# Kernel tuning notes

Hardware: AMD Instinct MI355X
Metric: run time of the kernel (lower is better)

Reference implementation:

```python
import jax, jax.numpy as jnp
import numpy as np

B, M, C, S, SD, K, H = 32, 448, 384, 512, 128, 8, 8
DH = C // H
EPS = 1e-5
NEG_SLOPE = 0.2


def setup_inputs() -> dict:
    key = jax.random.key(0)
    ks = iter(jax.random.split(key, 32))
    nrm = lambda shape, scale=0.05: (jax.random.normal(next(ks), shape, jnp.float32) * scale)
    inp = {
        'q': jax.random.normal(next(ks), (B, M, C), jnp.float32),
        'coarse': jax.random.normal(next(ks), (B, M, 3), jnp.float32),
        'skeleton': jax.random.normal(next(ks), (B, S, 3), jnp.float32),
        # GraphConv 1: 3 -> 64 (root weight, rel/neighbor weight, bias)
        'gc1_wroot': nrm((3, 64), 0.3), 'gc1_wrel': nrm((3, 64), 0.3), 'gc1_b': jnp.zeros((64,), jnp.float32),
        # GraphConv 2: 64 -> SD
        'gc2_wroot': nrm((64, SD), 0.1), 'gc2_wrel': nrm((64, SD), 0.1), 'gc2_b': jnp.zeros((SD,), jnp.float32),
        # skeleton_projection: SD -> C
        'proj_w': nrm((SD, C), 0.08), 'proj_b': jnp.zeros((C,), jnp.float32),
        # MultiheadAttention (torch layout: in_proj (3C, C), out_proj (C, C))
        'attn_in_w': nrm((3 * C, C), 0.05), 'attn_in_b': jnp.zeros((3 * C,), jnp.float32),
        'attn_out_w': nrm((C, C), 0.05), 'attn_out_b': jnp.zeros((C,), jnp.float32),
        # increase_dim: Conv1d(C,1024,1) + BN(1024) + LeakyReLU + Conv1d(1024,1024,1)
        'inc1_w': nrm((1024, C), 0.05), 'inc1_b': jnp.zeros((1024,), jnp.float32),
        'bn_g': jnp.ones((1024,), jnp.float32), 'bn_b': jnp.zeros((1024,), jnp.float32),
        'bn_m': jnp.zeros((1024,), jnp.float32), 'bn_v': jnp.ones((1024,), jnp.float32),
        'inc2_w': nrm((1024, 1024), 0.03), 'inc2_b': jnp.zeros((1024,), jnp.float32),
        # reduce_map: Linear(C + 1024 + 3, C)
        'red_w': nrm((1024 + C + 3, C), 0.03), 'red_b': jnp.zeros((C,), jnp.float32),
    }
    return inp


def _knn_idx(pts):
    # pts: [B,S,3]; per-batch kNN (self excluded), matching knn_graph(k=K, batch=...)
    d2 = jnp.sum((pts[:, :, None, :] - pts[:, None, :, :]) ** 2, axis=-1)  # [B,S,S]
    d2 = d2 + jnp.eye(S, dtype=pts.dtype)[None] * 1e10                       # mask self
    _, idx = jax.lax.top_k(-d2, K)                                           # [B,S,K]
    return idx


def _graph_conv(x, idx, wroot, wrel, b):
    # GraphConv (PyG, aggr='add'): out_i = x_i Wroot + (sum_{j in N(i)} x_j) Wrel + b
    nb = jax.vmap(lambda f, i: f[i])(x, idx)   # [B,S,K,F]
    agg = nb.sum(axis=2)                       # [B,S,F]
    return x @ wroot + agg @ wrel + b


def reference(q, coarse, skeleton, gc1_wroot, gc1_wrel, gc1_b, gc2_wroot, gc2_wrel, gc2_b,
              proj_w, proj_b, attn_in_w, attn_in_b, attn_out_w, attn_out_b,
              inc1_w, inc1_b, bn_g, bn_b, bn_m, bn_v, inc2_w, inc2_b, red_w, red_b):
    # --- skeleton branch: knn graph + 2-layer GraphConv + max-pool + projection ---
    idx = _knn_idx(skeleton)
    h = _graph_conv(skeleton, idx, gc1_wroot, gc1_wrel, gc1_b)
    h = jax.nn.relu(h)
    h = _graph_conv(h, idx, gc2_wroot, gc2_wrel, gc2_b)        # [B,S,SD]
    proxy = jnp.max(h, axis=1)                                  # [B,SD]
    proxy = proxy @ proj_w + proj_b                             # [B,C]
    kv = jnp.broadcast_to(proxy[:, None, :], (B, M, C))         # expanded proxies

    # --- cross attention (torch nn.MultiheadAttention math) ---
    wq, wk, wv = attn_in_w[:C], attn_in_w[C:2 * C], attn_in_w[2 * C:]
    bq, bk, bv = attn_in_b[:C], attn_in_b[C:2 * C], attn_in_b[2 * C:]
    qh = (q @ wq.T + bq).reshape(B, M, H, DH)
    kh = (kv @ wk.T + bk).reshape(B, M, H, DH)
    vh = (kv @ wv.T + bv).reshape(B, M, H, DH)
    scores = jnp.einsum('bmhd,bnhd->bhmn', qh, kh) / jnp.sqrt(jnp.float32(DH))
    attn = jax.nn.softmax(scores, axis=-1)
    ctx = jnp.einsum('bhmn,bnhd->bmhd', attn, vh).reshape(B, M, C)
    q = ctx @ attn_out_w.T + attn_out_b                         # fused features [B,M,C]

    # --- increase_dim (1x1 conv == matmul) + BN(eval) + LeakyReLU + 1x1 conv ---
    g = jnp.einsum('bmc,oc->bmo', q, inc1_w) + inc1_b           # [B,M,1024]
    g = bn_g * (g - bn_m) * jax.lax.rsqrt(bn_v + EPS) + bn_b
    g = jnp.where(g >= 0, g, NEG_SLOPE * g)
    g = jnp.einsum('bmc,oc->bmo', g, inc2_w) + inc2_b
    global_feature = jnp.max(g, axis=1)                         # [B,1024]

    # --- concat + reduce_map ---
    rebuild = jnp.concatenate([jnp.broadcast_to(global_feature[:, None, :], (B, M, 1024)), q, coarse], axis=-1)
    out = rebuild @ red_w + red_b                               # [B,M,C]
    return out
```

## Files before the change

kernel.cpp:

```cpp
#include <hip/hip_runtime.h>

#define NB 32
#define MM 448
#define CC 384
#define SS 512
#define KNN 8

#define WS_IDX   0u
#define WS_H1    524288u
#define WS_PMAX  (WS_H1 + 4194304u)
#define WS_Q     (WS_PMAX + 262144u)
#define WS_Y     (WS_Q + 49152u)
#define WS_G2    (WS_Y + 131072u)
#define WS_BASEP (WS_G2 + 131072u)
#define WS_PP    WS_H1

__device__ __forceinline__ float wave_sum(float v) {
#pragma unroll
  for (int m = 1; m < 64; m <<= 1) v += __shfl_xor(v, m, 64);
  return v;
}

__global__ __launch_bounds__(256) void k_knn_gc1(
    const float* __restrict__ skel,
    const float* __restrict__ w1root, const float* __restrict__ w1rel,
    const float* __restrict__ b1,
    int* __restrict__ idx_ws, float* __restrict__ h1_ws)
{
  int b   = blockIdx.x >> 7;
  int grp = blockIdx.x & 127;
  __shared__ __align__(16) float4 sk[SS];
  const float* sb = skel + b * SS * 3;
  for (int t = threadIdx.x; t < SS; t += 256)
    sk[t] = make_float4(sb[t*3+0], sb[t*3+1], sb[t*3+2], 0.f);
  __syncthreads();

  int wave = threadIdx.x >> 6, lane = threadIdx.x & 63;
  int i = grp * 4 + wave;
  float4 pi = sk[i];

  float bd[KNN];
#pragma unroll
  for (int t = 0; t < KNN; t++) {
    int j = lane + (t << 6);
    float4 p = sk[j];
    float d2;
    {
#pragma clang fp contract(off)
      float dx = pi.x - p.x, dy = pi.y - p.y, dz = pi.z - p.z;
      d2 = (dx*dx + dy*dy) + dz*dz;
    }
    bd[t] = (j == i) ? 3e38f : d2;
  }

  int win[KNN];
  int* idx_base = idx_ws + (size_t)(b*SS + i) * KNN;
#pragma unroll
  for (int t = 0; t < KNN; t++) {
    float bestd = bd[0]; int bests = 0;
#pragma unroll
    for (int s = 1; s < KNN; s++)
      if (bd[s] < bestd) { bestd = bd[s]; bests = s; }
    int bestj = lane + (bests << 6);
#pragma unroll
    for (int m = 1; m < 64; m <<= 1) {
      float od = __shfl_xor(bestd, m, 64);
      int   oj = __shfl_xor(bestj, m, 64);
      if (od < bestd || (od == bestd && oj < bestj)) { bestd = od; bestj = oj; }
    }
    win[t] = bestj;
    if (lane == t) idx_base[t] = bestj;
    if ((bestj & 63) == lane) {
      int sl = bestj >> 6;
#pragma unroll
      for (int s = 0; s < KNN; s++) if (s == sl) bd[s] = 3e38f;
    }
  }

  float a0 = 0.f, a1 = 0.f, a2 = 0.f;
#pragma unroll
  for (int t = 0; t < KNN; t++) {
    float4 n = sk[win[t]];
    a0 += n.x; a1 += n.y; a2 += n.z;
  }

  int c = lane;
  float h = b1[c] + pi.x*w1root[c] + pi.y*w1root[64+c] + pi.z*w1root[128+c]
                  + a0*w1rel[c]   + a1*w1rel[64+c]   + a2*w1rel[128+c];
  h = fmaxf(h, 0.f);
  h1_ws[(size_t)(b*SS + i) * 64 + lane] = h;
}

__global__ __launch_bounds__(256) void k_gc2_max(
    const float* __restrict__ h1_ws, const int* __restrict__ idx_ws,
    const float* __restrict__ w2root, const float* __restrict__ w2rel,
    const float* __restrict__ b2, float* __restrict__ pmax)
{
  int b = blockIdx.x >> 4, chunk = blockIdx.x & 15;
  int r0 = chunk * 32;
  __shared__ __align__(16) float X[32*129];
  __shared__ __align__(16) float Wt[32*128];
  __shared__ float mred[8*128];
  __shared__ int nbs[32*KNN];

  const float* h1b = h1_ws + (size_t)b * SS * 64;
  nbs[threadIdx.x] = idx_ws[(b*SS + r0)*KNN + threadIdx.x];
#pragma unroll
  for (int p = 0; p < 8; p++) {
    int idx = threadIdx.x + 256*p;
    int r = idx >> 6, k = idx & 63;
    X[r*129 + k] = h1b[(r0 + r)*64 + k];
  }
  __syncthreads();
#pragma unroll
  for (int p = 0; p < 8; p++) {
    int idx = threadIdx.x + 256*p;
    int r = idx >> 6, k = idx & 63;
    const int* nb = nbs + r*KNN;
    float s = 0.f;
#pragma unroll
    for (int j = 0; j < KNN; j++) s += h1b[nb[j]*64 + k];
    X[r*129 + 64 + k] = s;
  }

  int rg = threadIdx.x >> 5, cg = threadIdx.x & 31;
  float acc[4][4];
#pragma unroll
  for (int r = 0; r < 4; r++)
#pragma unroll
    for (int u = 0; u < 4; u++) acc[r][u] = 0.f;

  const float* wsrc[4] = { w2root, w2root + 32*128, w2rel, w2rel + 32*128 };
#pragma unroll 1
  for (int ch = 0; ch < 4; ch++) {
    __syncthreads();
    const float* ws = wsrc[ch];
#pragma unroll
    for (int p = 0; p < 16; p++) {
      int idx = threadIdx.x + 256*p;
      Wt[idx] = ws[idx];
    }
    __syncthreads();
    int kb = ch * 32;
    const float* xr0 = X + (rg*4+0)*129 + kb;
    const float* xr1 = X + (rg*4+1)*129 + kb;
    const float* xr2 = X + (rg*4+2)*129 + kb;
    const float* xr3 = X + (rg*4+3)*129 + kb;
#pragma unroll 4
    for (int k = 0; k < 32; k++) {
      float4 w4 = *(const float4*)(Wt + k*128 + cg*4);
      float x0 = xr0[k], x1 = xr1[k], x2 = xr2[k], x3 = xr3[k];
      acc[0][0] += x0*w4.x; acc[0][1] += x0*w4.y; acc[0][2] += x0*w4.z; acc[0][3] += x0*w4.w;
      acc[1][0] += x1*w4.x; acc[1][1] += x1*w4.y; acc[1][2] += x1*w4.z; acc[1][3] += x1*w4.w;
      acc[2][0] += x2*w4.x; acc[2][1] += x2*w4.y; acc[2][2] += x2*w4.z; acc[2][3] += x2*w4.w;
      acc[3][0] += x3*w4.x; acc[3][1] += x3*w4.y; acc[3][2] += x3*w4.z; acc[3][3] += x3*w4.w;
    }
  }
#pragma unroll
  for (int u = 0; u < 4; u++)
    mred[rg*128 + cg*4 + u] =
      fmaxf(fmaxf(acc[0][u], acc[1][u]), fmaxf(acc[2][u], acc[3][u]));
  __syncthreads();
  if (threadIdx.x < 128) {
    int col = threadIdx.x;
    float mx = mred[col];
#pragma unroll
    for (int g = 1; g < 8; g++) mx = fmaxf(mx, mred[g*128 + col]);
    pmax[(size_t)(b*16 + chunk)*128 + col] = mx + b2[col];
  }
}

__global__ __launch_bounds__(384) void k_attn_chain(
    const float* __restrict__ pmax,
    const float* __restrict__ proj_w, const float* __restrict__ proj_b,
    const float* __restrict__ attn_in_w, const float* __restrict__ attn_in_b,
    const float* __restrict__ attn_out_w, const float* __restrict__ attn_out_b,
    float* __restrict__ q_ws)
{
  int b = blockIdx.x, t = threadIdx.x;
  __shared__ float proxy[128];
  __shared__ float kv[CC];
  __shared__ float vv[CC];
  if (t < 128) {
    float m = -3e38f;
    for (int ch = 0; ch < 16; ch++) m = fmaxf(m, pmax[(size_t)(b*16 + ch)*128 + t]);
    proxy[t] = m;
  }
  __syncthreads();
  {
    float acc = proj_b[t];
    for (int s = 0; s < 128; s++) acc += proxy[s] * proj_w[s*CC + t];
    kv[t] = acc;
  }
  __syncthreads();
  int wv = t >> 6, lane = t & 63;
  {
    float x0 = kv[lane*6+0], x1 = kv[lane*6+1], x2 = kv[lane*6+2];
    float x3 = kv[lane*6+3], x4 = kv[lane*6+4], x5 = kv[lane*6+5];
#pragma unroll 8
    for (int u = 0; u < 64; u++) {
      int o = wv*64 + u;
      const float* wr = attn_in_w + (size_t)(2*CC + o) * CC + lane*6;
      float2 wa = *(const float2*)wr;
      float2 wb = *(const float2*)(wr + 2);
      float2 wc = *(const float2*)(wr + 4);
      float p = wa.x*x0 + wa.y*x1 + wb.x*x2 + wb.y*x3 + wc.x*x4 + wc.y*x5;
      p = wave_sum(p);
      if (lane == 0) vv[o] = attn_in_b[2*CC + o] + p;
    }
  }
  __syncthreads();
  {
    float x0 = vv[lane*6+0], x1 = vv[lane*6+1], x2 = vv[lane*6+2];
    float x3 = vv[lane*6+3], x4 = vv[lane*6+4], x5 = vv[lane*6+5];
#pragma unroll 8
    for (int u = 0; u < 64; u++) {
      int o = wv*64 + u;
      const float* wr = attn_out_w + (size_t)o * CC + lane*6;
      float2 wa = *(const float2*)wr;
      float2 wb = *(const float2*)(wr + 2);
      float2 wc = *(const float2*)(wr + 4);
      float p = wa.x*x0 + wa.y*x1 + wb.x*x2 + wb.y*x3 + wc.x*x4 + wc.y*x5;
      p = wave_sum(p);
      if (lane == 0) q_ws[b*CC + o] = attn_out_b[o] + p;
    }
  }
}

__global__ __launch_bounds__(256) void k_inc1_bn(
    const float* __restrict__ q_ws, const float* __restrict__ inc1_w,
    const float* __restrict__ inc1_b,
    const float* __restrict__ bng, const float* __restrict__ bnb,
    const float* __restrict__ bnm, const float* __restrict__ bnv,
    float* __restrict__ y_ws)
{
  int b = blockIdx.x >> 5, og = blockIdx.x & 31;
  int wv = threadIdx.x >> 6, lane = threadIdx.x & 63;
  __shared__ float xs[CC];
  for (int t = threadIdx.x; t < CC; t += 256) xs[t] = q_ws[b*CC + t];
  __syncthreads();
  float x0 = xs[lane*6+0], x1 = xs[lane*6+1], x2 = xs[lane*6+2];
  float x3 = xs[lane*6+3], x4 = xs[lane*6+4], x5 = xs[lane*6+5];
#pragma unroll
  for (int u = 0; u < 8; u++) {
    int o = og*32 + wv*8 + u;
    const float* wr = inc1_w + (size_t)o * CC + lane*6;
    float2 wa = *(const float2*)wr;
    float2 wb = *(const float2*)(wr + 2);
    float2 wc = *(const float2*)(wr + 4);
    float p = wa.x*x0 + wa.y*x1 + wb.x*x2 + wb.y*x3 + wc.x*x4 + wc.y*x5;
    p = wave_sum(p);
    if (lane == 0) {
      float acc = p + inc1_b[o];
      float z = bng[o] * (acc - bnm[o]) * rsqrtf(bnv[o] + 1e-5f) + bnb[o];
      y_ws[b*1024 + o] = (z >= 0.f) ? z : 0.2f * z;
    }
  }
}

__global__ __launch_bounds__(256) void k_inc2(
    const float* __restrict__ y_ws, const float* __restrict__ inc2_w,
    const float* __restrict__ inc2_b, float* __restrict__ g2_ws)
{
  int b = blockIdx.x >> 5, og = blockIdx.x & 31;
  int wv = threadIdx.x >> 6, lane = threadIdx.x & 63;
  __shared__ __align__(16) float xs[1024];
  for (int t = threadIdx.x; t < 1024; t += 256) xs[t] = y_ws[b*1024 + t];
  __syncthreads();
  float4 X0 = *(const float4*)(xs + lane*16 + 0);
  float4 X1 = *(const float4*)(xs + lane*16 + 4);
  float4 X2 = *(const float4*)(xs + lane*16 + 8);
  float4 X3 = *(const float4*)(xs + lane*16 + 12);
#pragma unroll
  for (int u = 0; u < 8; u++) {
    int o = og*32 + wv*8 + u;
    const float* wr = inc2_w + (size_t)o * 1024 + lane*16;
    float4 W0 = *(const float4*)(wr + 0);
    float4 W1 = *(const float4*)(wr + 4);
    float4 W2 = *(const float4*)(wr + 8);
    float4 W3 = *(const float4*)(wr + 12);
    float p = W0.x*X0.x + W0.y*X0.y + W0.z*X0.z + W0.w*X0.w
            + W1.x*X1.x + W1.y*X1.y + W1.z*X1.z + W1.w*X1.w
            + W2.x*X2.x + W2.y*X2.y + W2.z*X2.z + W2.w*X2.w
            + W3.x*X3.x + W3.y*X3.y + W3.z*X3.z + W3.w*X3.w;
    p = wave_sum(p);
    if (lane == 0) g2_ws[b*1024 + o] = p + inc2_b[o];
  }
}

__global__ __launch_bounds__(256) void k_basep(
    const float* __restrict__ g2_ws, const float* __restrict__ q_ws,
    const float* __restrict__ red_w, float* __restrict__ pp)
{
  int cg = blockIdx.x;
  int o0 = blockIdx.y * 64;
  int c0 = cg * 32;
  __shared__ __align__(16) float xs[32*33];
  __shared__ __align__(16) float wt[32*64];
#pragma unroll
  for (int p = 0; p < 8; p++) {
    int idx = threadIdx.x + 256*p;
    int c = idx >> 6, o = idx & 63;
    wt[idx] = red_w[(size_t)(c0 + c)*CC + o0 + o];
  }
  {
    int b = threadIdx.x >> 3, cp = threadIdx.x & 7;
    const float* src = (cg < 32) ? (g2_ws + b*1024 + c0)
                                 : (q_ws  + b*CC   + (c0 - 1024));
    float4 v = *(const float4*)(src + cp*4);
    xs[(cp*4+0)*33 + b] = v.x;
    xs[(cp*4+1)*33 + b] = v.y;
    xs[(cp*4+2)*33 + b] = v.z;
    xs[(cp*4+3)*33 + b] = v.w;
  }
  __syncthreads();
  int b = threadIdx.x >> 3, og = threadIdx.x & 7;
  float acc[8];
#pragma unroll
  for (int u = 0; u < 8; u++) acc[u] = 0.f;
#pragma unroll 8
  for (int c = 0; c < 32; c++) {
    float xv = xs[c*33 + b];
    float4 w0 = *(const float4*)(wt + c*64 + og*8);
    float4 w1 = *(const float4*)(wt + c*64 + og*8 + 4);
    acc[0] += xv*w0.x; acc[1] += xv*w0.y; acc[2] += xv*w0.z; acc[3] += xv*w0.w;
    acc[4] += xv*w1.x; acc[5] += xv*w1.y; acc[6] += xv*w1.z; acc[7] += xv*w1.w;
  }
  float* dst = pp + (size_t)(cg*32 + b)*CC + o0 + og*8;
  *(float4*)dst       = make_float4(acc[0], acc[1], acc[2], acc[3]);
  *(float4*)(dst + 4) = make_float4(acc[4], acc[5], acc[6], acc[7]);
}

__global__ __launch_bounds__(256) void k_base_red(
    const float* __restrict__ pp, float* __restrict__ basep)
{
  int idx = blockIdx.x * 256 + threadIdx.x;
  float s = 0.f;
#pragma unroll 4
  for (int cg = 0; cg < 44; cg++) s += pp[cg*12288 + idx];
  basep[idx] = s;
}

__global__ __launch_bounds__(256) void k_out(
    const float* __restrict__ basep, const float* __restrict__ red_b,
    const float* __restrict__ red_w, const float* __restrict__ coarse,
    float* __restrict__ out)
{
  int gid = blockIdx.x * 256 + threadIdx.x;
  int c4 = gid % 96;
  int row = gid / 96;
  int b = row / 448;
  int c = c4 * 4;
  float4 p0 = *(const float4*)(basep + b*CC + c);
  float4 rb = *(const float4*)(red_b + c);
  const float* cr = coarse + (size_t)row * 3;
  float cx = cr[0], cy = cr[1], cz = cr[2];
  float4 w0 = *(const float4*)(red_w + (size_t)1408*CC + c);
  float4 w1 = *(const float4*)(red_w + (size_t)1409*CC + c);
  float4 w2 = *(const float4*)(red_w + (size_t)1410*CC + c);
  float4 o4;
  o4.x = p0.x + rb.x + cx*w0.x + cy*w1.x + cz*w2.x;
  o4.y = p0.y + rb.y + cx*w0.y + cy*w1.y + cz*w2.y;
  o4.z = p0.z + rb.z + cx*w0.z + cy*w1.z + cz*w2.z;
  o4.w = p0.w + rb.w + cx*w0.w + cy*w1.w + cz*w2.w;
  *(float4*)(out + (size_t)row*CC + c) = o4;
}

extern "C" void kernel_launch(void* const* d_in, const int* in_sizes, int n_in,
                              void* d_out, int out_size, void* d_ws, size_t ws_size,
                              hipStream_t stream)
{
  (void)in_sizes; (void)n_in; (void)out_size; (void)ws_size;
  const float* coarse = (const float*)d_in[1];
  const float* skel   = (const float*)d_in[2];
  const float* g1wr   = (const float*)d_in[3];
  const float* g1wl   = (const float*)d_in[4];
  const float* g1b    = (const float*)d_in[5];
  const float* g2wr   = (const float*)d_in[6];
  const float* g2wl   = (const float*)d_in[7];
  const float* g2b    = (const float*)d_in[8];
  const float* projw  = (const float*)d_in[9];
  const float* projb  = (const float*)d_in[10];
  const float* aiw    = (const float*)d_in[11];
  const float* aib    = (const float*)d_in[12];
  const float* aow    = (const float*)d_in[13];
  const float* aob    = (const float*)d_in[14];
  const float* i1w    = (const float*)d_in[15];
  const float* i1b    = (const float*)d_in[16];
  const float* bng    = (const float*)d_in[17];
  const float* bnb    = (const float*)d_in[18];
  const float* bnm    = (const float*)d_in[19];
  const float* bnv    = (const float*)d_in[20];
  const float* i2w    = (const float*)d_in[21];
  const float* i2b    = (const float*)d_in[22];
  const float* redw   = (const float*)d_in[23];
  const float* redb   = (const float*)d_in[24];
  float* out = (float*)d_out;

  char* ws = (char*)d_ws;
  int*   idx_ws = (int*)(ws + WS_IDX);
  float* h1_ws  = (float*)(ws + WS_H1);
  float* pmax   = (float*)(ws + WS_PMAX);
  float* q_ws   = (float*)(ws + WS_Q);
  float* y_ws   = (float*)(ws + WS_Y);
  float* g2_ws  = (float*)(ws + WS_G2);
  float* basep  = (float*)(ws + WS_BASEP);
  float* pp     = (float*)(ws + WS_PP);

  k_knn_gc1<<<4096, 256, 0, stream>>>(skel, g1wr, g1wl, g1b, idx_ws, h1_ws);
  k_gc2_max<<<512, 256, 0, stream>>>(h1_ws, idx_ws, g2wr, g2wl, g2b, pmax);
  k_attn_chain<<<32, 384, 0, stream>>>(pmax, projw, projb, aiw, aib, aow, aob, q_ws);
  k_inc1_bn<<<1024, 256, 0, stream>>>(q_ws, i1w, i1b, bng, bnb, bnm, bnv, y_ws);
  k_inc2<<<1024, 256, 0, stream>>>(y_ws, i2w, i2b, g2_ws);
  k_basep<<<dim3(44, 6), 256, 0, stream>>>(g2_ws, q_ws, redw, pp);
  k_base_red<<<48, 256, 0, stream>>>(pp, basep);
  k_out<<<5376, 256, 0, stream>>>(basep, redb, redw, coarse, out);
}
```

Baseline: 292.0 us.

## Split attention chain into parallel matvec kernels and restructure inc1/inc2 matvecs

The single 32-block attention chain kernel, which serially ran the V projection and output projection per batch, is split into a proxy/kv kernel plus two generic 384-wide matvec launches with 384 blocks each. This spreads the weight reads across many more CUs. The inc1 and inc2 matvecs are also reorganized: each output is computed by 4 threads doing float4 dot products over a quarter of K, reduced with two shuffles instead of a full 64-lane wave reduction, using half as many blocks. The cost is two extra launches and extra workspace round-trips for the kv and vv vectors, which are stored in the idx region that is no longer needed at that point.

After: 234.2 us. 19.8% less time.

```diff
diff --git a/kernel.cpp b/kernel.cpp
--- a/kernel.cpp
+++ b/kernel.cpp
@@ -14,6 +14,8 @@
 #define WS_G2    (WS_Y + 131072u)
 #define WS_BASEP (WS_G2 + 131072u)
 #define WS_PP    WS_H1
+#define WS_KV    WS_IDX
+#define WS_VV    (WS_IDX + 49152u)
 
 __device__ __forceinline__ float wave_sum(float v) {
 #pragma unroll
@@ -170,60 +172,45 @@
   }
 }
 
-__global__ __launch_bounds__(384) void k_attn_chain(
+__global__ __launch_bounds__(384) void k_proxy_kv(
     const float* __restrict__ pmax,
     const float* __restrict__ proj_w, const float* __restrict__ proj_b,
-    const float* __restrict__ attn_in_w, const float* __restrict__ attn_in_b,
-    const float* __restrict__ attn_out_w, const float* __restrict__ attn_out_b,
-    float* __restrict__ q_ws)
+    float* __restrict__ kv_ws)
 {
   int b = blockIdx.x, t = threadIdx.x;
   __shared__ float proxy[128];
-  __shared__ float kv[CC];
-  __shared__ float vv[CC];
   if (t < 128) {
     float m = -3e38f;
     for (int ch = 0; ch < 16; ch++) m = fmaxf(m, pmax[(size_t)(b*16 + ch)*128 + t]);
     proxy[t] = m;
   }
   __syncthreads();
-  {
-    float acc = proj_b[t];
-    for (int s = 0; s < 128; s++) acc += proxy[s] * proj_w[s*CC + t];
-    kv[t] = acc;
-  }
-  __syncthreads();
-  int wv = t >> 6, lane = t & 63;
-  {
-    float x0 = kv[lane*6+0], x1 = kv[lane*6+1], x2 = kv[lane*6+2];
-    float x3 = kv[lane*6+3], x4 = kv[lane*6+4], x5 = kv[lane*6+5];
-#pragma unroll 8
-    for (int u = 0; u < 64; u++) {
-      int o = wv*64 + u;
-      const float* wr = attn_in_w + (size_t)(2*CC + o) * CC + lane*6;
-      float2 wa = *(const float2*)wr;
-      float2 wb = *(const float2*)(wr + 2);
-      float2 wc = *(const float2*)(wr + 4);
-      float p = wa.x*x0 + wa.y*x1 + wb.x*x2 + wb.y*x3 + wc.x*x4 + wc.y*x5;
-      p = wave_sum(p);
-      if (lane == 0) vv[o] = attn_in_b[2*CC + o] + p;
-    }
-  }
-  __syncthreads();
-  {
-    float x0 = vv[lane*6+0], x1 = vv[lane*6+1], x2 = vv[lane*6+2];
-    float x3 = vv[lane*6+3], x4 = vv[lane*6+4], x5 = vv[lane*6+5];
-#pragma unroll 8
-    for (int u = 0; u < 64; u++) {
-      int o = wv*64 + u;
-      const float* wr = attn_out_w + (size_t)o * CC + lane*6;
-      float2 wa = *(const float2*)wr;
-      float2 wb = *(const float2*)(wr + 2);
-      float2 wc = *(const float2*)(wr + 4);
-      float p = wa.x*x0 + wa.y*x1 + wb.x*x2 + wb.y*x3 + wc.x*x4 + wc.y*x5;
-      p = wave_sum(p);
-      if (lane == 0) q_ws[b*CC + o] = attn_out_b[o] + p;
-    }
+  float acc = proj_b[t];
+  for (int s = 0; s < 128; s++) acc += proxy[s] * proj_w[s*CC + t];
+  kv_ws[b*CC + t] = acc;
+}
+
+__global__ __launch_bounds__(256) void k_mv384(
+    const float* __restrict__ xin, const float* __restrict__ w, int row0,
+    const float* __restrict__ bias, int bias0, float* __restrict__ out)
+{
+  int b = blockIdx.x, og = blockIdx.y;
+  int wv = threadIdx.x >> 6, lane = threadIdx.x & 63;
+  __shared__ float xs[CC];
+  for (int t = threadIdx.x; t < CC; t += 256) xs[t] = xin[b*CC + t];
+  __syncthreads();
+  float x0 = xs[lane*6+0], x1 = xs[lane*6+1], x2 = xs[lane*6+2];
+  float x3 = xs[lane*6+3], x4 = xs[lane*6+4], x5 = xs[lane*6+5];
+#pragma unroll
+  for (int u = 0; u < 8; u++) {
+    int o = og*32 + wv*8 + u;
+    const float* wr = w + (size_t)(row0 + o) * CC + lane*6;
+    float2 wa = *(const float2*)wr;
+    float2 wb = *(const float2*)(wr + 2);
+    float2 wc = *(const float2*)(wr + 4);
+    float p = wa.x*x0 + wa.y*x1 + wb.x*x2 + wb.y*x3 + wc.x*x4 + wc.y*x5;
+    p = wave_sum(p);
+    if (lane == 0) out[b*CC + o] = bias[bias0 + o] + p;
   }
 }
 
@@ -234,27 +221,27 @@
     const float* __restrict__ bnm, const float* __restrict__ bnv,
     float* __restrict__ y_ws)
 {
-  int b = blockIdx.x >> 5, og = blockIdx.x & 31;
-  int wv = threadIdx.x >> 6, lane = threadIdx.x & 63;
-  __shared__ float xs[CC];
-  for (int t = threadIdx.x; t < CC; t += 256) xs[t] = q_ws[b*CC + t];
-  __syncthreads();
-  float x0 = xs[lane*6+0], x1 = xs[lane*6+1], x2 = xs[lane*6+2];
-  float x3 = xs[lane*6+3], x4 = xs[lane*6+4], x5 = xs[lane*6+5];
-#pragma unroll
-  for (int u = 0; u < 8; u++) {
-    int o = og*32 + wv*8 + u;
-    const float* wr = inc1_w + (size_t)o * CC + lane*6;
-    float2 wa = *(const float2*)wr;
-    float2 wb = *(const float2*)(wr + 2);
-    float2 wc = *(const float2*)(wr + 4);
-    float p = wa.x*x0 + wa.y*x1 + wb.x*x2 + wb.y*x3 + wc.x*x4 + wc.y*x5;
-    p = wave_sum(p);
-    if (lane == 0) {
-      float acc = p + inc1_b[o];
-      float z = bng[o] * (acc - bnm[o]) * rsqrtf(bnv[o] + 1e-5f) + bnb[o];
-      y_ws[b*1024 + o] = (z >= 0.f) ? z : 0.2f * z;
-    }
+  int b = blockIdx.x >> 4, og = blockIdx.x & 15;
+  int t = threadIdx.x;
+  int o = og*64 + (t >> 2), qq = t & 3;
+  __shared__ __align__(16) float xs[CC];
+  for (int i = t; i < CC; i += 256) xs[i] = q_ws[b*CC + i];
+  __syncthreads();
+  const float* wr = inc1_w + (size_t)o * CC + qq*96;
+  const float* xr = xs + qq*96;
+  float acc = 0.f;
+#pragma unroll
+  for (int kk = 0; kk < 96; kk += 4) {
+    float4 w4 = *(const float4*)(wr + kk);
+    float4 x4 = *(const float4*)(xr + kk);
+    acc += w4.x*x4.x + w4.y*x4.y + w4.z*x4.z + w4.w*x4.w;
+  }
+  acc += __shfl_xor(acc, 1, 64);
+  acc += __shfl_xor(acc, 2, 64);
+  if (qq == 0) {
+    float a = acc + inc1_b[o];
+    float z = bng[o] * (a - bnm[o]) * rsqrtf(bnv[o] + 1e-5f) + bnb[o];
+    y_ws[b*1024 + o] = (z >= 0.f) ? z : 0.2f * z;
   }
 }
 
@@ -262,30 +249,24 @@
     const float* __restrict__ y_ws, const float* __restrict__ inc2_w,
     const float* __restrict__ inc2_b, float* __restrict__ g2_ws)
 {
-  int b = blockIdx.x >> 5, og = blockIdx.x & 31;
-  int wv = threadIdx.x >> 6, lane = threadIdx.x & 63;
+  int b = blockIdx.x >> 4, og = blockIdx.x & 15;
+  int t = threadIdx.x;
+  int o = og*64 + (t >> 2), qq = t & 3;
   __shared__ __align__(16) float xs[1024];
-  for (int t = threadIdx.x; t < 1024; t += 256) xs[t] = y_ws[b*1024 + t];
-  __syncthreads();
-  float4 X0 = *(const float4*)(xs + lane*16 + 0);
-  float4 X1 = *(const float4*)(xs + lane*16 + 4);
-  float4 X2 = *(const float4*)(xs + lane*16 + 8);
-  float4 X3 = *(const float4*)(xs + lane*16 + 12);
-#pragma unroll
-  for (int u = 0; u < 8; u++) {
-    int o = og*32 + wv*8 + u;
-    const float* wr = inc2_w + (size_t)o * 1024 + lane*16;
-    float4 W0 = *(const float4*)(wr + 0);
-    float4 W1 = *(const float4*)(wr + 4);
-    float4 W2 = *(const float4*)(wr + 8);
-    float4 W3 = *(const float4*)(wr + 12);
-    float p = W0.x*X0.x + W0.y*X0.y + W0.z*X0.z + W0.w*X0.w
-            + W1.x*X1.x + W1.y*X1.y + W1.z*X1.z + W1.w*X1.w
-            + W2.x*X2.x + W2.y*X2.y + W2.z*X2.z + W2.w*X2.w
-            + W3.x*X3.x + W3.y*X3.y + W3.z*X3.z + W3.w*X3.w;
-    p = wave_sum(p);
-    if (lane == 0) g2_ws[b*1024 + o] = p + inc2_b[o];
-  }
+  for (int i = t; i < 1024; i += 256) xs[i] = y_ws[b*1024 + i];
+  __syncthreads();
+  const float* wr = inc2_w + (size_t)o * 1024 + qq*256;
+  const float* xr = xs + qq*256;
+  float acc = 0.f;
+#pragma unroll 8
+  for (int kk = 0; kk < 256; kk += 4) {
+    float4 w4 = *(const float4*)(wr + kk);
+    float4 x4 = *(const float4*)(xr + kk);
+    acc += w4.x*x4.x + w4.y*x4.y + w4.z*x4.z + w4.w*x4.w;
+  }
+  acc += __shfl_xor(acc, 1, 64);
+  acc += __shfl_xor(acc, 2, 64);
+  if (qq == 0) g2_ws[b*1024 + o] = acc + inc2_b[o];
 }
 
 __global__ __launch_bounds__(256) void k_basep(
@@ -406,12 +387,16 @@
   float* g2_ws  = (float*)(ws + WS_G2);
   float* basep  = (float*)(ws + WS_BASEP);
   float* pp     = (float*)(ws + WS_PP);
+  float* kv_ws  = (float*)(ws + WS_KV);
+  float* vv_ws  = (float*)(ws + WS_VV);
 
   k_knn_gc1<<<4096, 256, 0, stream>>>(skel, g1wr, g1wl, g1b, idx_ws, h1_ws);
   k_gc2_max<<<512, 256, 0, stream>>>(h1_ws, idx_ws, g2wr, g2wl, g2b, pmax);
-  k_attn_chain<<<32, 384, 0, stream>>>(pmax, projw, projb, aiw, aib, aow, aob, q_ws);
-  k_inc1_bn<<<1024, 256, 0, stream>>>(q_ws, i1w, i1b, bng, bnb, bnm, bnv, y_ws);
-  k_inc2<<<1024, 256, 0, stream>>>(y_ws, i2w, i2b, g2_ws);
+  k_proxy_kv<<<32, 384, 0, stream>>>(pmax, projw, projb, kv_ws);
+  k_mv384<<<dim3(32, 12), 256, 0, stream>>>(kv_ws, aiw, 2*CC, aib, 2*CC, vv_ws);
+  k_mv384<<<dim3(32, 12), 256, 0, stream>>>(vv_ws, aow, 0,    aob, 0,    q_ws);
+  k_inc1_bn<<<512, 256, 0, stream>>>(q_ws, i1w, i1b, bng, bnb, bnm, bnv, y_ws);
+  k_inc2<<<512, 256, 0, stream>>>(y_ws, i2w, i2b, g2_ws);
   k_basep<<<dim3(44, 6), 256, 0, stream>>>(g2_ws, q_ws, redw, pp);
   k_base_red<<<48, 256, 0, stream>>>(pp, basep);
   k_out<<<5376, 256, 0, stream>>>(basep, redb, redw, coarse, out);
```
